# Kernel tuning notes

Measured on AMD Instinct MI355X. Metric: run time of the kernel, lower is better.

Reference implementation:

```python
import jax, jax.numpy as jnp
import numpy as np

ALPHA = 0.2  # LeakyReLU negative slope
NEG_INF = -9e15


def setup_inputs() -> dict:
    key = jax.random.key(0)
    k1, k2, k3, k4 = jax.random.split(key, 4)
    B, N, Fin, Fout = 4, 4096, 256, 128
    h = jax.random.normal(k1, (B, N, Fin), dtype=jnp.float32)
    adj = jax.random.randint(k2, (B, N, N), 0, 2, dtype=jnp.int32)  # {0,1} adjacency
    # xavier_uniform with gain 1.414
    limW = 1.414 * np.sqrt(6.0 / (Fin + Fout))
    W = jax.random.uniform(k3, (Fin, Fout), jnp.float32, -limW, limW)
    lima = 1.414 * np.sqrt(6.0 / (2 * Fout + 1))
    a = jax.random.uniform(k4, (2 * Fout, 1), jnp.float32, -lima, lima)
    return {"h": h, "adj": adj, "W": W, "a": a}


def reference(h, adj, W, a):
    # Wh: [B, N, Fout]
    Wh = jnp.einsum('bni,io->bno', h, W)
    Fout = W.shape[1]
    # Decompose a^T [Wh_i || Wh_j] = a1.Wh_i + a2.Wh_j (identical math, avoids
    # materializing the [B,N,N,2F] concat tensor the torch code builds).
    a1, a2 = a[:Fout, 0], a[Fout:, 0]
    s1 = jnp.einsum('bno,o->bn', Wh, a1)  # [B, N]
    s2 = jnp.einsum('bno,o->bn', Wh, a2)  # [B, N]
    e = jax.nn.leaky_relu(s1[:, :, None] + s2[:, None, :], negative_slope=ALPHA)  # [B,N,N]
    attention = jnp.where(adj > 0, e, jnp.asarray(NEG_INF, e.dtype))
    attention = jax.nn.softmax(attention, axis=2)
    # dropout is inactive in eval mode (training=False)
    # Faithful to the torch code: the FIRST h_prime is overwritten; the output is
    # einsum('bjk,bji->bki', attention, Wh) -> sums over the softmax (row) axis j.
    h_prime = jnp.einsum('bjk,bji->bki', attention, Wh)  # [B, N, Fout]
    return jax.nn.elu(h_prime)  # concat=True
```

## Files before the change

kernel.cpp:

```cpp
#include <hip/hip_runtime.h>
#include <hip/hip_bf16.h>

#define ALPHA 0.2f
#define L2E 1.4426950408889634f

constexpr int Nn = 4096;
constexpr int FIN = 256;
constexpr int FOUT = 128;
constexpr int JC = 4;
constexpr int JQ = 1024;
constexpr int NCH = 32;
constexpr long long SLAB = 2097152;

typedef __attribute__((ext_vector_type(8))) short short8;
typedef __attribute__((ext_vector_type(8))) unsigned short ushort8;
typedef __attribute__((ext_vector_type(4))) float f32x4;
typedef __attribute__((ext_vector_type(16))) float f32x16;
typedef __attribute__((ext_vector_type(4))) int int4v;

__device__ __forceinline__ unsigned short f2bf(float x) {
  unsigned int u = __float_as_uint(x);
  unsigned int r = (u + 0x7fffu + ((u >> 16) & 1u)) >> 16;
  return (unsigned short)r;
}

__device__ __forceinline__ float bf2f(unsigned short v) {
  return __uint_as_float(((unsigned)v) << 16);
}

__device__ __forceinline__ void gload16(const void* g, void* l) {
  auto lp = (__attribute__((address_space(3))) void*)l;
  auto gp = (const __attribute__((address_space(1))) void*)g;
  __builtin_amdgcn_global_load_lds(gp, lp, 16, 0, 0);
}

__global__ __launch_bounds__(256) void k0_prep(
    const float* __restrict__ W, unsigned short* __restrict__ WT) {
  __shared__ float lw[32][132];
  int t = threadIdx.x;
  int kc0 = blockIdx.x * 32;
#pragma unroll
  for (int m = 0; m < 4; ++m) {
    int idx = t * 16 + m * 4;
    f32x4 v = *(const f32x4*)(W + kc0 * 128 + idx);
    int k = idx >> 7, i0 = idx & 127;
    *(f32x4*)&lw[k][i0] = v;
  }
  __syncthreads();
  int i = t >> 1, half = t & 1;
  unsigned short pk[16];
#pragma unroll
  for (int kk = 0; kk < 16; ++kk) pk[kk] = f2bf(lw[half * 16 + kk][i]);
  ushort8* dst = (ushort8*)(WT + i * 256 + kc0 + half * 16);
  dst[0] = *(ushort8*)&pk[0];
  dst[1] = *(ushort8*)&pk[8];
}

__global__ __launch_bounds__(256) void k1b_wh(
    const float* __restrict__ h, const unsigned short* __restrict__ WT,
    const float* __restrict__ a, unsigned short* __restrict__ whT,
    float* __restrict__ s1L, float* __restrict__ s2L) {
  __shared__ __align__(16) char smem[36864];
  int t = threadIdx.x;
  int w = t >> 6, l = t & 63, g = l >> 4, r = l & 15;
  int r0 = blockIdx.x * 16;
  int b = r0 >> 12, nbase = r0 & 4095;

  f32x4 acc[2];
  acc[0] = (f32x4){0.f, 0.f, 0.f, 0.f};
  acc[1] = (f32x4){0.f, 0.f, 0.f, 0.f};

  for (int kc = 0; kc < 2; ++kc) {
    __syncthreads();
    {
      int row = t >> 4, sec = t & 15;
      const f32x4* src =
          (const f32x4*)(h + (long long)(r0 + row) * 256 + kc * 128 + sec * 8);
      f32x4 v0 = src[0], v1 = src[1];
      unsigned int pk[4];
      pk[0] = ((unsigned)f2bf(v0.y) << 16) | f2bf(v0.x);
      pk[1] = ((unsigned)f2bf(v0.w) << 16) | f2bf(v0.z);
      pk[2] = ((unsigned)f2bf(v1.y) << 16) | f2bf(v1.x);
      pk[3] = ((unsigned)f2bf(v1.w) << 16) | f2bf(v1.z);
      *(ushort8*)(smem + row * 256 + ((sec ^ (row & 7)) << 4)) = *(ushort8*)pk;
    }
    {
      int i = t >> 1, pt = t & 1;
      const ushort8* src = (const ushort8*)(WT + i * 256 + kc * 128 + pt * 64);
#pragma unroll
      for (int m = 0; m < 8; ++m) {
        ushort8 v = src[m];
        int slot = pt * 8 + m;
        *(ushort8*)(smem + 4096 + i * 256 + ((slot ^ (i & 7)) << 4)) = v;
      }
    }
    __syncthreads();
#pragma unroll
    for (int kk = 0; kk < 4; ++kk) {
      short8 af =
          *(const short8*)(smem + r * 256 + (((kk * 4 + g) ^ (r & 7)) << 4));
#pragma unroll
      for (int s = 0; s < 2; ++s) {
        int i = w * 32 + s * 16 + r;
        short8 bf = *(const short8*)(smem + 4096 + i * 256 +
                                     (((kk * 4 + g) ^ (i & 7)) << 4));
        acc[s] =
            __builtin_amdgcn_mfma_f32_16x16x32_bf16(af, bf, acc[s], 0, 0, 0);
      }
    }
  }

  __syncthreads();
  unsigned short* tb = (unsigned short*)smem;
#pragma unroll
  for (int s = 0; s < 2; ++s)
#pragma unroll
    for (int q = 0; q < 4; ++q)
      tb[(w * 32 + s * 16 + r) * 25 + g * 4 + q] = f2bf(acc[s][q]);
  __syncthreads();

  {
    int i = t >> 1, half = t & 1;
    ushort8 v = *(const ushort8*)(tb + i * 25 + half * 8);
    *(ushort8*)(whT + (((long long)(b * 128 + i)) << 12) + nbase + half * 8) =
        v;
  }
  {
    int n = t >> 4, seg = t & 15;
    f32x4 a10 = *(const f32x4*)(a + seg * 8);
    f32x4 a11 = *(const f32x4*)(a + seg * 8 + 4);
    f32x4 a20 = *(const f32x4*)(a + 128 + seg * 8);
    f32x4 a21 = *(const f32x4*)(a + 128 + seg * 8 + 4);
    float v1 = 0.f, v2 = 0.f;
#pragma unroll
    for (int m = 0; m < 8; ++m) {
      float wh = bf2f(tb[(seg * 8 + m) * 25 + n]);
      float c1 = (m < 4) ? a10[m] : a11[m - 4];
      float c2 = (m < 4) ? a20[m] : a21[m - 4];
      v1 += wh * c1;
      v2 += wh * c2;
    }
#pragma unroll
    for (int off = 8; off; off >>= 1) {
      v1 += __shfl_xor(v1, off);
      v2 += __shfl_xor(v2, off);
    }
    if (seg == 0) {
      s1L[r0 + n] = v1 * L2E;
      s2L[r0 + n] = v2 * L2E;
    }
  }
}

__global__ __launch_bounds__(256) void k2_stats(
    const int* __restrict__ adj, const float* __restrict__ s1L,
    const float* __restrict__ s2L, float2* __restrict__ st2,
    unsigned long long* __restrict__ mask64) {
  __shared__ unsigned int mwords[2][128];
  __shared__ float wsum[2][4];
  int row0 = blockIdx.x * 2;
  int b = row0 >> 12;
  int t = threadIdx.x;
  float s1a = s1L[row0];
  float s1b = s1L[row0 + 1];
  const int4v* arow0 = (const int4v*)(adj + (long long)row0 * Nn);
  const int4v* arow1 = (const int4v*)(adj + (long long)(row0 + 1) * Nn);
  const f32x4* s2v = (const f32x4*)(s2L + (b << 12));

  float sumA = 0.f, sumB = 0.f;
#pragma unroll
  for (int q = 0; q < 4; ++q) {
    int4v av0 = arow0[q * 256 + t];
    int4v av1 = arow1[q * 256 + t];
    f32x4 sv = s2v[q * 256 + t];
    unsigned nibA = 0, nibB = 0;
#pragma unroll
    for (int c = 0; c < 4; ++c) {
      float uA = s1a + sv[c];
      float uB = s1b + sv[c];
      float vA = fmaxf(uA, ALPHA * uA);
      float vB = fmaxf(uB, ALPHA * uB);
      sumA = fmaf((float)av0[c], exp2f(vA), sumA);
      sumB = fmaf((float)av1[c], exp2f(vB), sumB);
      nibA |= ((unsigned)av0[c]) << c;
      nibB |= ((unsigned)av1[c]) << c;
    }
    unsigned a1 = nibA | (__shfl_xor(nibA, 1) << 4);
    unsigned a2 = a1 | (__shfl_xor(a1, 2) << 8);
    unsigned a4 = a2 | (__shfl_xor(a2, 4) << 16);
    unsigned b1 = nibB | (__shfl_xor(nibB, 1) << 4);
    unsigned b2 = b1 | (__shfl_xor(b1, 2) << 8);
    unsigned b4 = b2 | (__shfl_xor(b2, 4) << 16);
    if ((t & 7) == 0) {
      mwords[0][q * 32 + (t >> 3)] = a4;
      mwords[1][q * 32 + (t >> 3)] = b4;
    }
  }
#pragma unroll
  for (int off = 32; off; off >>= 1) {
    sumA += __shfl_xor(sumA, off);
    sumB += __shfl_xor(sumB, off);
  }
  if ((t & 63) == 0) {
    wsum[0][t >> 6] = sumA;
    wsum[1][t >> 6] = sumB;
  }
  __syncthreads();
  if (t < 128) {
    int rr = t >> 6, idx = t & 63;
    unsigned long long mv = *(unsigned long long*)&mwords[rr][idx * 2];
    mask64[((long long)(row0 + rr) << 6) + idx] = mv;
  }
  if (t < 2) {
    float S = wsum[t][0] + wsum[t][1] + wsum[t][2] + wsum[t][3];
    float negc = (S > 0.f) ? -log2f(S) : -1.0e30f;
    float s1 = (t == 0) ? s1a : s1b;
    st2[row0 + t] = make_float2(s1 + negc, ALPHA * s1 + negc);
  }
}

__global__ __launch_bounds__(512, 4) void k3_pv(
    const unsigned short* __restrict__ whT, const float2* __restrict__ st2,
    const unsigned long long* __restrict__ mask64,
    const float* __restrict__ s2L, unsigned short* __restrict__ pbuf) {
  __shared__ __align__(16) char smem[40960];
  char* mbase = smem + 16384;
  float2* stl = (float2*)(smem + 32768);

  int t = threadIdx.x;
  int orig = blockIdx.x;
  int x = orig & 7, mm = orig >> 3;
  int b = x >> 1;
  int kt = ((x & 1) << 4) | (mm & 15);
  int jc = mm >> 4;
  int w = t >> 6, l = t & 63, hl = l >> 5, ln = l & 31;
  int ks = w & 3, jh = w >> 2;
  int jq0 = jc * JQ;
  long long brow = (long long)(b << 12);
  int k0 = kt << 7;
  float z1 = s2L[brow + k0 + ks * 32 + ln];
  float z2 = ALPHA * z1;
  int sh31 = 31 - ln;

  gload16(st2 + brow + jq0 + t * 2, (char*)stl + t * 16);
  {
    const char* m0 =
        (const char*)(mask64 + ((brow + jq0 + t) << 6)) + kt * 16;
    const char* m1 =
        (const char*)(mask64 + ((brow + jq0 + 512 + t) << 6)) + kt * 16;
    gload16(m0, mbase + t * 16);
    gload16(m1, mbase + 8192 + t * 16);
  }
  const unsigned short* whTb = whT + ((long long)b << 19);
  int joct0 = t >> 7, gi = t & 127;
  const unsigned short* wsrc0 =
      whTb + (long long)gi * 4096 + jq0 + joct0 * 8;
  gload16(wsrc0, smem + t * 16);
  __syncthreads();

  f32x16 acc[4];
#pragma unroll
  for (int q = 0; q < 4; ++q)
#pragma unroll
    for (int r = 0; r < 16; ++r) acc[q][r] = 0.f;

  for (int ch = 0; ch < NCH; ++ch) {
    int cur = ch & 1;
    if (ch + 1 < NCH)
      gload16(wsrc0 + (ch + 1) * 32, smem + (cur ^ 1) * 8192 + t * 16);
    char* wb = smem + cur * 8192;
    int jb = ch * 32 + jh * 16 + hl * 8;
    short8 af;
#pragma unroll
    for (int e = 0; e < 8; ++e) {
      int ja = jb + e;
      float2 sc = stl[ja];
      unsigned int mv = *(unsigned int*)(mbase + ja * 16 + ks * 4);
      float e1 = sc.x + z1;
      float e2 = sc.y + z2;
      float p = exp2f(fmaxf(e1, e2));
      int msk = ((int)(mv << sh31)) >> 31;
      unsigned pu = __float_as_uint(p) & (unsigned)msk;
      __hip_bfloat16 hb = __float2bfloat16(__uint_as_float(pu));
      af[e] = *(short*)&hb;
    }
    int gb = (jh * 2 + hl) * 2048;
#pragma unroll
    for (int q = 0; q < 4; ++q) {
      short8 bv = *(const short8*)(wb + gb + ((q * 32 + ln) << 4));
      acc[q] = __builtin_amdgcn_mfma_f32_32x32x16_bf16(af, bv, acc[q], 0, 0, 0);
    }
    __syncthreads();
  }

  unsigned short* zone = (unsigned short*)smem;
  if (jh == 1) {
#pragma unroll
    for (int q = 0; q < 4; ++q)
#pragma unroll
      for (int r = 0; r < 16; ++r) {
        int kl = (r & 3) + ((r >> 2) << 3) + (hl << 2);
        zone[ks * 4096 + q * 1024 + kl * 32 + ln] = f2bf(acc[q][r]);
      }
  }
  __syncthreads();
  if (jh == 0) {
    unsigned short* pb = pbuf + (long long)jc * SLAB + ((brow + k0) << 7);
#pragma unroll
    for (int q = 0; q < 4; ++q)
#pragma unroll
      for (int r = 0; r < 16; ++r) {
        int kl = (r & 3) + ((r >> 2) << 3) + (hl << 2);
        float v = acc[q][r] + bf2f(zone[ks * 4096 + q * 1024 + kl * 32 + ln]);
        pb[(ks * 32 + kl) * 128 + q * 32 + ln] = f2bf(v);
      }
  }
}

__global__ __launch_bounds__(256) void k4_reduce(
    const unsigned short* __restrict__ pbuf, float* __restrict__ out) {
  int orig = blockIdx.x;
  int n = (orig & 7) * 128 + (orig >> 3);
  int base = (n * 256 + threadIdx.x) * 8;
  float s[8] = {0.f, 0.f, 0.f, 0.f, 0.f, 0.f, 0.f, 0.f};
#pragma unroll
  for (int sl = 0; sl < JC; ++sl) {
    ushort8 v = *(const ushort8*)(pbuf + (long long)sl * SLAB + base);
#pragma unroll
    for (int e = 0; e < 8; ++e)
      s[e] += __uint_as_float(((unsigned)(unsigned short)v[e]) << 16);
  }
  f32x4 o0, o1;
#pragma unroll
  for (int e = 0; e < 8; ++e) {
    float xv = s[e];
    float y = xv > 0.f ? xv : expm1f(xv);
    if (e < 4) o0[e] = y; else o1[e - 4] = y;
  }
  *(f32x4*)(out + base) = o0;
  *(f32x4*)(out + base + 4) = o1;
}

extern "C" void kernel_launch(void* const* d_in, const int* in_sizes, int n_in,
                              void* d_out, int out_size, void* d_ws,
                              size_t ws_size, hipStream_t stream) {
  const float* h = (const float*)d_in[0];
  const int* adj = (const int*)d_in[1];
  const float* W = (const float*)d_in[2];
  const float* a = (const float*)d_in[3];
  float* out = (float*)d_out;

  char* ws = (char*)d_ws;
  unsigned short* WT = (unsigned short*)ws;
  unsigned short* whT = (unsigned short*)(ws + (1 << 20));
  float* s1L = (float*)(ws + (5 << 20));
  float* s2L = s1L + 16384;
  float2* st2 = (float2*)(ws + (5 << 20) + (128 << 10));
  unsigned long long* mask64 =
      (unsigned long long*)(ws + (6 << 20));
  unsigned short* pbuf = (unsigned short*)(ws + (16 << 20));

  hipLaunchKernelGGL(k0_prep, dim3(8), dim3(256), 0, stream, W, WT);
  hipLaunchKernelGGL(k1b_wh, dim3(1024), dim3(256), 0, stream, h, WT, a, whT,
                     s1L, s2L);
  hipLaunchKernelGGL(k2_stats, dim3(8192), dim3(256), 0, stream, adj, s1L,
                     s2L, st2, mask64);
  hipLaunchKernelGGL(k3_pv, dim3(512), dim3(512), 0, stream, whT, st2, mask64,
                     s2L, pbuf);
  hipLaunchKernelGGL(k4_reduce, dim3(1024), dim3(256), 0, stream, pbuf, out);
}
```

Before: 125.3 us.

## Split j range finer and fuse final reduction into PV kernel via atomic counter

Doubles the number of j-chunks so the PV kernel launches twice as many blocks, each covering half the j range. The separate reduce+ELU kernel is removed: the last block per (batch, k-tile) to finish, found with an atomic counter reset in the prep kernel, sums the bf16 partial slabs and writes the ELU output. Mask words are now staged in a planar LDS layout and read with vector loads. The changes aim to raise parallelism and cut one launch, in exchange for twice the partial-buffer traffic and a serialized tail reduction in the last-arriving blocks.

```diff
diff --git a/kernel.cpp b/kernel.cpp
--- a/kernel.cpp
+++ b/kernel.cpp
@@ -7,9 +7,9 @@
 constexpr int Nn = 4096;
 constexpr int FIN = 256;
 constexpr int FOUT = 128;
-constexpr int JC = 4;
-constexpr int JQ = 1024;
-constexpr int NCH = 32;
+constexpr int JC = 8;
+constexpr int JQ = 512;
+constexpr int NCH = 16;
 constexpr long long SLAB = 2097152;
 
 typedef __attribute__((ext_vector_type(8))) short short8;
@@ -17,6 +17,7 @@
 typedef __attribute__((ext_vector_type(4))) float f32x4;
 typedef __attribute__((ext_vector_type(16))) float f32x16;
 typedef __attribute__((ext_vector_type(4))) int int4v;
+typedef __attribute__((ext_vector_type(4))) unsigned int uint4v;
 
 __device__ __forceinline__ unsigned short f2bf(float x) {
   unsigned int u = __float_as_uint(x);
@@ -35,9 +36,11 @@
 }
 
 __global__ __launch_bounds__(256) void k0_prep(
-    const float* __restrict__ W, unsigned short* __restrict__ WT) {
+    const float* __restrict__ W, unsigned short* __restrict__ WT,
+    int* __restrict__ cnt) {
   __shared__ float lw[32][132];
   int t = threadIdx.x;
+  if (blockIdx.x == 0 && t < 128) cnt[t] = 0;
   int kc0 = blockIdx.x * 32;
 #pragma unroll
   for (int m = 0; m < 4; ++m) {
@@ -222,10 +225,11 @@
 __global__ __launch_bounds__(512, 4) void k3_pv(
     const unsigned short* __restrict__ whT, const float2* __restrict__ st2,
     const unsigned long long* __restrict__ mask64,
-    const float* __restrict__ s2L, unsigned short* __restrict__ pbuf) {
+    const float* __restrict__ s2L, unsigned short* __restrict__ pbuf,
+    int* __restrict__ cnt, float* __restrict__ out) {
   __shared__ __align__(16) char smem[40960];
-  char* mbase = smem + 16384;
-  float2* stl = (float2*)(smem + 32768);
+  unsigned int* mkpl = (unsigned int*)(smem + 16384);
+  float2* stl = (float2*)(smem + 24576);
 
   int t = threadIdx.x;
   int orig = blockIdx.x;
@@ -242,19 +246,19 @@
   float z2 = ALPHA * z1;
   int sh31 = 31 - ln;
 
-  gload16(st2 + brow + jq0 + t * 2, (char*)stl + t * 16);
+  if (t < 256) gload16(st2 + brow + jq0 + t * 2, (char*)stl + t * 16);
   {
-    const char* m0 =
-        (const char*)(mask64 + ((brow + jq0 + t) << 6)) + kt * 16;
-    const char* m1 =
-        (const char*)(mask64 + ((brow + jq0 + 512 + t) << 6)) + kt * 16;
-    gload16(m0, mbase + t * 16);
-    gload16(m1, mbase + 8192 + t * 16);
+    uint4v mrow = *(const uint4v*)((const char*)(mask64 +
+                                                 ((brow + jq0 + t) << 6)) +
+                                   kt * 16);
+    mkpl[0 * 512 + t] = mrow[0];
+    mkpl[1 * 512 + t] = mrow[1];
+    mkpl[2 * 512 + t] = mrow[2];
+    mkpl[3 * 512 + t] = mrow[3];
   }
   const unsigned short* whTb = whT + ((long long)b << 19);
-  int joct0 = t >> 7, gi = t & 127;
-  const unsigned short* wsrc0 =
-      whTb + (long long)gi * 4096 + jq0 + joct0 * 8;
+  int gi = t & 127;
+  const unsigned short* wsrc0 = whTb + (long long)gi * 4096 + jq0 + (t >> 7) * 8;
   gload16(wsrc0, smem + t * 16);
   __syncthreads();
 
@@ -264,18 +268,20 @@
 #pragma unroll
     for (int r = 0; r < 16; ++r) acc[q][r] = 0.f;
 
+  const unsigned int* mkw = mkpl + ks * 512;
   for (int ch = 0; ch < NCH; ++ch) {
     int cur = ch & 1;
     if (ch + 1 < NCH)
       gload16(wsrc0 + (ch + 1) * 32, smem + (cur ^ 1) * 8192 + t * 16);
     char* wb = smem + cur * 8192;
     int jb = ch * 32 + jh * 16 + hl * 8;
+    uint4v mw0 = *(const uint4v*)(mkw + jb);
+    uint4v mw1 = *(const uint4v*)(mkw + jb + 4);
     short8 af;
 #pragma unroll
     for (int e = 0; e < 8; ++e) {
-      int ja = jb + e;
-      float2 sc = stl[ja];
-      unsigned int mv = *(unsigned int*)(mbase + ja * 16 + ks * 4);
+      float2 sc = stl[jb + e];
+      unsigned mv = (e < 4) ? mw0[e] : mw1[e - 4];
       float e1 = sc.x + z1;
       float e2 = sc.y + z2;
       float p = exp2f(fmaxf(e1, e2));
@@ -304,8 +310,9 @@
       }
   }
   __syncthreads();
+  long long rbase = (brow + k0) << 7;
   if (jh == 0) {
-    unsigned short* pb = pbuf + (long long)jc * SLAB + ((brow + k0) << 7);
+    unsigned short* pb = pbuf + (long long)jc * SLAB + rbase;
 #pragma unroll
     for (int q = 0; q < 4; ++q)
 #pragma unroll
@@ -315,30 +322,35 @@
         pb[(ks * 32 + kl) * 128 + q * 32 + ln] = f2bf(v);
       }
   }
-}
-
-__global__ __launch_bounds__(256) void k4_reduce(
-    const unsigned short* __restrict__ pbuf, float* __restrict__ out) {
-  int orig = blockIdx.x;
-  int n = (orig & 7) * 128 + (orig >> 3);
-  int base = (n * 256 + threadIdx.x) * 8;
-  float s[8] = {0.f, 0.f, 0.f, 0.f, 0.f, 0.f, 0.f, 0.f};
-#pragma unroll
-  for (int sl = 0; sl < JC; ++sl) {
-    ushort8 v = *(const ushort8*)(pbuf + (long long)sl * SLAB + base);
-#pragma unroll
-    for (int e = 0; e < 8; ++e)
-      s[e] += __uint_as_float(((unsigned)(unsigned short)v[e]) << 16);
-  }
-  f32x4 o0, o1;
-#pragma unroll
-  for (int e = 0; e < 8; ++e) {
-    float xv = s[e];
-    float y = xv > 0.f ? xv : expm1f(xv);
-    if (e < 4) o0[e] = y; else o1[e - 4] = y;
-  }
-  *(f32x4*)(out + base) = o0;
-  *(f32x4*)(out + base + 4) = o1;
+
+  __threadfence();
+  __syncthreads();
+  int* flag = (int*)(smem + 40000);
+  if (t == 0) *flag = (atomicAdd(&cnt[b * 32 + kt], 1) == JC - 1) ? 1 : 0;
+  __syncthreads();
+  if (*flag) {
+    __threadfence();
+#pragma unroll
+    for (int m = 0; m < 4; ++m) {
+      int idx = m * 4096 + t * 8;
+      float s[8] = {0.f, 0.f, 0.f, 0.f, 0.f, 0.f, 0.f, 0.f};
+#pragma unroll
+      for (int sl = 0; sl < JC; ++sl) {
+        ushort8 v = *(const ushort8*)(pbuf + (long long)sl * SLAB + rbase + idx);
+#pragma unroll
+        for (int e = 0; e < 8; ++e) s[e] += bf2f((unsigned short)v[e]);
+      }
+      f32x4 o0, o1;
+#pragma unroll
+      for (int e = 0; e < 8; ++e) {
+        float xv = s[e];
+        float y = xv > 0.f ? xv : expm1f(xv);
+        if (e < 4) o0[e] = y; else o1[e - 4] = y;
+      }
+      *(f32x4*)(out + rbase + idx) = o0;
+      *(f32x4*)(out + rbase + idx + 4) = o1;
+    }
+  }
 }
 
 extern "C" void kernel_launch(void* const* d_in, const int* in_sizes, int n_in,
@@ -356,16 +368,16 @@
   float* s1L = (float*)(ws + (5 << 20));
   float* s2L = s1L + 16384;
   float2* st2 = (float2*)(ws + (5 << 20) + (128 << 10));
+  int* cnt = (int*)(ws + (5 << 20) + (512 << 10));
   unsigned long long* mask64 =
       (unsigned long long*)(ws + (6 << 20));
   unsigned short* pbuf = (unsigned short*)(ws + (16 << 20));
 
-  hipLaunchKernelGGL(k0_prep, dim3(8), dim3(256), 0, stream, W, WT);
+  hipLaunchKernelGGL(k0_prep, dim3(8), dim3(256), 0, stream, W, WT, cnt);
   hipLaunchKernelGGL(k1b_wh, dim3(1024), dim3(256), 0, stream, h, WT, a, whT,
                      s1L, s2L);
   hipLaunchKernelGGL(k2_stats, dim3(8192), dim3(256), 0, stream, adj, s1L,
                      s2L, st2, mask64);
-  hipLaunchKernelGGL(k3_pv, dim3(512), dim3(512), 0, stream, whT, st2, mask64,
-                     s2L, pbuf);
-  hipLaunchKernelGGL(k4_reduce, dim3(1024), dim3(256), 0, stream, pbuf, out);
-}
+  hipLaunchKernelGGL(k3_pv, dim3(1024), dim3(512), 0, stream, whT, st2,
+                     mask64, s2L, pbuf, cnt, out);
+}
```

Result: slower. 332.1 us (+165.1%).
